# Kernel optimization log

Measured on AMD Instinct MI355X. Metric: run time of the kernel, lower is better.

The kernel has to match this reference:

```python
import jax, jax.numpy as jnp
import numpy as np

N_NODES = 100000
F_STATE = 64
HIDDEN = 256
N_EDGES = 1600000


def setup_inputs() -> dict:
    key = jax.random.key(0)
    ks = jax.random.split(key, 8)
    x = jax.random.normal(ks[0], (N_NODES, F_STATE), dtype=jnp.float32)
    edge_index = jax.random.randint(ks[1], (2, N_EDGES), 0, N_NODES, dtype=jnp.int32)
    # Pre-process MLP (1 layer): Dense(F_STATE -> HIDDEN), relu
    W_pre = jax.random.normal(ks[2], (F_STATE, HIDDEN), dtype=jnp.float32) / np.sqrt(F_STATE)
    b_pre = jnp.zeros((HIDDEN,), dtype=jnp.float32)
    # GeneralConv: Dense(HIDDEN -> HIDDEN), relu, then sum-aggregate message passing
    W_conv = jax.random.normal(ks[3], (HIDDEN, HIDDEN), dtype=jnp.float32) / np.sqrt(HIDDEN)
    b_conv = jnp.zeros((HIDDEN,), dtype=jnp.float32)
    # Post-process MLP (1 layer): Dense(2*HIDDEN -> F_STATE), activation=None
    W_post = jax.random.normal(ks[4], (2 * HIDDEN, F_STATE), dtype=jnp.float32) / np.sqrt(2 * HIDDEN)
    b_post = jnp.zeros((F_STATE,), dtype=jnp.float32)
    return {
        "x": x,
        "edge_index": edge_index,
        "W_pre": W_pre,
        "b_pre": b_pre,
        "W_conv": W_conv,
        "b_conv": b_conv,
        "W_post": W_post,
        "b_post": b_post,
        "steps": 4,
    }


def reference(x, edge_index, W_pre, b_pre, W_conv, b_conv, W_post, b_post, steps):
    n = x.shape[0]
    dst = edge_index[0]  # a.indices[:, 0] -> aggregation targets
    src = edge_index[1]  # a.indices[:, 1] -> message sources

    def step(h, _):
        p = jax.nn.relu(h @ W_pre + b_pre)                 # pre MLP     [N, H]
        m = jax.nn.relu(p @ W_conv + b_conv)               # conv dense  [N, H]
        z = jax.ops.segment_sum(m[src], dst, num_segments=n)  # sum agg  [N, H]
        out = jnp.concatenate([z, p], axis=-1) @ W_post + b_post  # cat-skip + post MLP (linear)
        return out, None

    out, _ = jax.lax.scan(step, x, None, length=steps)
    return out
```

## Files before the change

### kernel.cpp

```cpp
#include <hip/hip_runtime.h>


#define NN 100000
#define NPAD 100064
#define FS 64
#define HH 256
#define NE 1600000
#define NSTEPS 4
#define GA 128
#define EPB (NE / GA)
#define BK2SH 9
#define BS2 (1 << BK2SH)
#define NBK2 ((NN + BS2 - 1) / BS2)

typedef unsigned short u16;
typedef unsigned int u32;
typedef __attribute__((ext_vector_type(8))) short bfrag;
typedef __attribute__((ext_vector_type(4))) float ffrag;

static __device__ __forceinline__ u16 f2bf(float f) {
    union { float f; u32 u; } v; v.f = f;
    return (u16)((v.u + 0x7fffu + ((v.u >> 16) & 1u)) >> 16);
}
static __device__ __forceinline__ float bf2f(u16 h) {
    union { u32 u; float f; } v; v.u = (u32)h << 16; return v.f;
}
static __device__ __forceinline__ u32 pack2bf(float a, float b) {
    return (u32)f2bf(a) | ((u32)f2bf(b) << 16);
}

__global__ void cvt_x_k(const float4* __restrict__ x, uint2* __restrict__ hbf, int n4) {
    int i = blockIdx.x * 256 + threadIdx.x;
    if (i < n4) {
        float4 v = x[i];
        hbf[i] = make_uint2(pack2bf(v.x, v.y), pack2bf(v.z, v.w));
    }
}

__global__ void prep_w_k(const float* __restrict__ W_pre, const float* __restrict__ W_conv,
                         const float* __restrict__ W_post,
                         u16* __restrict__ Wpt, u16* __restrict__ Wct,
                         u16* __restrict__ Wzt, u16* __restrict__ Wp2t) {
    int i = blockIdx.x * 256 + threadIdx.x;
    if (i < 65536) {
        int c = i >> 8, k = i & 255;
        Wct[i] = f2bf(W_conv[k * HH + c]);
    } else if (i < 81920) {
        int j = i - 65536;
        int c = j >> 6, k = j & 63;
        Wpt[j] = f2bf(W_pre[k * HH + c]);
    } else if (i < 98304) {
        int j = i - 81920;
        int c = j >> 8, k = j & 255;
        Wzt[j] = f2bf(W_post[k * FS + c]);
    } else if (i < 114688) {
        int j = i - 98304;
        int c = j >> 8, k = j & 255;
        Wp2t[j] = f2bf(W_post[(HH + k) * FS + c]);
    }
}

__global__ __launch_bounds__(256) void fillA_k(const int* __restrict__ dst, const int* __restrict__ src,
                                               int* __restrict__ cntM, int* __restrict__ offM,
                                               u32* __restrict__ tmp) {
    __shared__ int cnt[256];
    __shared__ int sc[256];
    __shared__ int cur[256];
    const int t = threadIdx.x, b = blockIdx.x;
    const int e0 = b * EPB;
    cnt[t] = 0;
    __syncthreads();
    for (int i = t; i < EPB; i += 256) atomicAdd(&cnt[dst[e0 + i] >> BK2SH], 1);
    __syncthreads();
    int v = cnt[t];
    sc[t] = v;
    __syncthreads();
    for (int o = 1; o < 256; o <<= 1) {
        int y = (t >= o) ? sc[t - o] : 0;
        __syncthreads();
        sc[t] += y;
        __syncthreads();
    }
    int excl = sc[t] - v;
    cur[t] = excl;
    if (t < NBK2) {
        cntM[t * GA + b] = v;
        offM[t * GA + b] = excl;
    }
    __syncthreads();
    u32* seg = tmp + (size_t)b * EPB;
    for (int i = t; i < EPB; i += 256) {
        int d = dst[e0 + i], s = src[e0 + i];
        int pos = atomicAdd(&cur[d >> BK2SH], 1);
        seg[pos] = ((u32)(d & (BS2 - 1)) << 23) | (u32)s;
    }
}

__global__ void bscan_k(const int* __restrict__ cntM, int* __restrict__ bstart) {
    __shared__ int sh[256];
    const int t = threadIdx.x;
    int tot = 0;
    if (t < NBK2)
        for (int b = 0; b < GA; b++) tot += cntM[t * GA + b];
    sh[t] = tot;
    __syncthreads();
    for (int o = 1; o < 256; o <<= 1) {
        int y = (t >= o) ? sh[t - o] : 0;
        __syncthreads();
        sh[t] += y;
        __syncthreads();
    }
    if (t < NBK2) bstart[t] = sh[t] - tot;
    if (t == 255) bstart[NBK2] = sh[255];
}

__global__ __launch_bounds__(256) void fillB_k(const u32* __restrict__ tmp,
                                               const int* __restrict__ cntM, const int* __restrict__ offM,
                                               const int* __restrict__ bstart,
                                               int* __restrict__ offsets, int* __restrict__ srcs) {
    __shared__ int cnt[BS2];
    __shared__ int cur[BS2];
    __shared__ int runlen[GA];
    __shared__ int runoff[GA];
    const int t = threadIdx.x, k = blockIdx.x;
    const int nodeBase = k << BK2SH;
    cnt[t] = 0;
    cnt[t + 256] = 0;
    if (t < GA) {
        runlen[t] = cntM[k * GA + t];
        runoff[t] = offM[k * GA + t];
    }
    __syncthreads();
    const int rsub = t >> 6;
    const int elane = t & 63;
    for (int g = 0; g < GA / 4; g++) {
        int rb = g * 4 + rsub;
        int len = runlen[rb];
        const u32* run = tmp + (size_t)rb * EPB + runoff[rb];
        for (int e = elane; e < len; e += 64) atomicAdd(&cnt[run[e] >> 23], 1);
    }
    __syncthreads();
    int a = cnt[2 * t], b2 = cnt[2 * t + 1];
    int s = a + b2;
    cur[t] = s;
    __syncthreads();
    for (int o = 1; o < 256; o <<= 1) {
        int y = (t >= o) ? cur[t - o] : 0;
        __syncthreads();
        cur[t] += y;
        __syncthreads();
    }
    int exclPair = cur[t] - s;
    __syncthreads();
    const int base = bstart[k];
    int o0 = base + exclPair;
    int o1 = o0 + a;
    int n0 = nodeBase + 2 * t, n1 = n0 + 1;
    if (n0 < NN) offsets[n0] = o0;
    if (n1 < NN) offsets[n1] = o1;
    cur[2 * t] = o0;
    cur[2 * t + 1] = o1;
    __syncthreads();
    for (int g = 0; g < GA / 4; g++) {
        int rb = g * 4 + rsub;
        int len = runlen[rb];
        const u32* run = tmp + (size_t)rb * EPB + runoff[rb];
        for (int e = elane; e < len; e += 64) {
            u32 p = run[e];
            int pos = atomicAdd(&cur[p >> 23], 1);
            srcs[pos] = (int)(p & 0x7FFFFFu);
        }
    }
}

__global__ void final_off_k(int* __restrict__ offsets) {
    if (threadIdx.x == 0) offsets[NN] = NE;
}

__global__ __launch_bounds__(256, 4) void xform_k(const u16* __restrict__ hbf,
                                                  const u16* __restrict__ Wpt,
                                                  const float* __restrict__ b_pre,
                                                  const u16* __restrict__ Wct,
                                                  const float* __restrict__ b_conv,
                                                  const u16* __restrict__ Wzt,
                                                  const u16* __restrict__ Wp2t,
                                                  u16* __restrict__ qbf,
                                                  float* __restrict__ pw2o) {
    __shared__ u16 ts[64 * 264];
    const int t = threadIdx.x;
    const int wave = t >> 6, lane = t & 63;
    const int quad = lane >> 4, l16 = lane & 15;
    const int nodeBase = blockIdx.x * 64;

    {
        ffrag acc[4][4];
#pragma unroll
        for (int mt = 0; mt < 4; mt++)
#pragma unroll
            for (int nt = 0; nt < 4; nt++) acc[mt][nt] = (ffrag)0.f;
#pragma unroll
        for (int ch = 0; ch < 2; ch++) {
            const int kb = ch * 32 + quad * 8;
            bfrag a[4], b[4];
#pragma unroll
            for (int mt = 0; mt < 4; mt++)
                a[mt] = *(const bfrag*)(hbf + (size_t)(nodeBase + mt * 16 + l16) * FS + kb);
#pragma unroll
            for (int nt = 0; nt < 4; nt++)
                b[nt] = *(const bfrag*)(Wpt + (size_t)(wave * 64 + nt * 16 + l16) * FS + kb);
#pragma unroll
            for (int mt = 0; mt < 4; mt++)
#pragma unroll
                for (int nt = 0; nt < 4; nt++)
                    acc[mt][nt] = __builtin_amdgcn_mfma_f32_16x16x32_bf16(a[mt], b[nt], acc[mt][nt], 0, 0, 0);
        }
#pragma unroll
        for (int nt = 0; nt < 4; nt++) {
            const int col = wave * 64 + nt * 16 + l16;
            const float bv = b_pre[col];
#pragma unroll
            for (int mt = 0; mt < 4; mt++)
#pragma unroll
                for (int r = 0; r < 4; r++)
                    ts[(mt * 16 + quad * 4 + r) * 264 + col] = f2bf(fmaxf(acc[mt][nt][r] + bv, 0.f));
        }
    }
    __syncthreads();

    ffrag accm[4][4];
    ffrag accw[4];
    {
#pragma unroll
        for (int mt = 0; mt < 4; mt++) {
            accw[mt] = (ffrag)0.f;
#pragma unroll
            for (int nt = 0; nt < 4; nt++) accm[mt][nt] = (ffrag)0.f;
        }
#pragma unroll
        for (int ch = 0; ch < 8; ch++) {
            const int kb = ch * 32 + quad * 8;
            bfrag a[4], b[4], bw;
#pragma unroll
            for (int mt = 0; mt < 4; mt++)
                a[mt] = *(const bfrag*)(ts + (mt * 16 + l16) * 264 + kb);
#pragma unroll
            for (int nt = 0; nt < 4; nt++)
                b[nt] = *(const bfrag*)(Wct + (size_t)(wave * 64 + nt * 16 + l16) * HH + kb);
            bw = *(const bfrag*)(Wp2t + (size_t)(wave * 16 + l16) * HH + kb);
#pragma unroll
            for (int mt = 0; mt < 4; mt++) {
#pragma unroll
                for (int nt = 0; nt < 4; nt++)
                    accm[mt][nt] = __builtin_amdgcn_mfma_f32_16x16x32_bf16(a[mt], b[nt], accm[mt][nt], 0, 0, 0);
                accw[mt] = __builtin_amdgcn_mfma_f32_16x16x32_bf16(a[mt], bw, accw[mt], 0, 0, 0);
            }
        }
    }
    __syncthreads();

    {
#pragma unroll
        for (int nt = 0; nt < 4; nt++) {
            const int col = wave * 64 + nt * 16 + l16;
            const float bv = b_conv[col];
#pragma unroll
            for (int mt = 0; mt < 4; mt++)
#pragma unroll
                for (int r = 0; r < 4; r++)
                    ts[(mt * 16 + quad * 4 + r) * 264 + col] = f2bf(fmaxf(accm[mt][nt][r] + bv, 0.f));
        }
        const int colw = wave * 16 + l16;
#pragma unroll
        for (int mt = 0; mt < 4; mt++)
#pragma unroll
            for (int r = 0; r < 4; r++) {
                int node = nodeBase + mt * 16 + quad * 4 + r;
                if (node < NN) pw2o[(size_t)node * FS + colw] = accw[mt][r];
            }
    }
    __syncthreads();

    {
        ffrag qa[4];
#pragma unroll
        for (int mt = 0; mt < 4; mt++) qa[mt] = (ffrag)0.f;
#pragma unroll
        for (int ch = 0; ch < 8; ch++) {
            const int kb = ch * 32 + quad * 8;
            bfrag bz = *(const bfrag*)(Wzt + (size_t)(wave * 16 + l16) * HH + kb);
#pragma unroll
            for (int mt = 0; mt < 4; mt++) {
                bfrag am = *(const bfrag*)(ts + (mt * 16 + l16) * 264 + kb);
                qa[mt] = __builtin_amdgcn_mfma_f32_16x16x32_bf16(am, bz, qa[mt], 0, 0, 0);
            }
        }
        const int col = wave * 16 + l16;
#pragma unroll
        for (int mt = 0; mt < 4; mt++)
#pragma unroll
            for (int r = 0; r < 4; r++) {
                int node = nodeBase + mt * 16 + quad * 4 + r;
                if (node < NN) qbf[(size_t)node * FS + col] = f2bf(qa[mt][r]);
            }
    }
}

__global__ __launch_bounds__(256) void agg_k(const u32* __restrict__ q2,
                                             const int* __restrict__ offsets,
                                             const int* __restrict__ srcs,
                                             const float* __restrict__ pw2,
                                             const float* __restrict__ b_post,
                                             u32* __restrict__ hbf_out,
                                             float* __restrict__ outf) {
    const int wave = threadIdx.x >> 6;
    const int lane = threadIdx.x & 63;
    const int node = blockIdx.x * 4 + wave;
    const int half = lane >> 5, c = lane & 31;
    const int beg = offsets[node], end = offsets[node + 1];
    float ax = 0.f, ay = 0.f, bx = 0.f, by = 0.f;
    int e = beg + half;
    for (; e + 6 < end; e += 8) {
        int s0 = srcs[e], s1 = srcs[e + 2], s2 = srcs[e + 4], s3 = srcs[e + 6];
        u32 g0 = q2[(size_t)s0 * 32 + c];
        u32 g1 = q2[(size_t)s1 * 32 + c];
        u32 g2 = q2[(size_t)s2 * 32 + c];
        u32 g3 = q2[(size_t)s3 * 32 + c];
        ax += bf2f((u16)g0) + bf2f((u16)g1);
        ay += bf2f((u16)(g0 >> 16)) + bf2f((u16)(g1 >> 16));
        bx += bf2f((u16)g2) + bf2f((u16)g3);
        by += bf2f((u16)(g2 >> 16)) + bf2f((u16)(g3 >> 16));
    }
    for (; e < end; e += 2) {
        u32 g = q2[(size_t)srcs[e] * 32 + c];
        ax += bf2f((u16)g);
        ay += bf2f((u16)(g >> 16));
    }
    ax += bx; ay += by;
    ax += __shfl_xor(ax, 32);
    ay += __shfl_xor(ay, 32);
    if (half == 0) {
        float2 w = *(const float2*)&pw2[(size_t)node * FS + 2 * c];
        float2 b = *(const float2*)&b_post[2 * c];
        float hx = ax + w.x + b.x;
        float hy = ay + w.y + b.y;
        if (outf) {
            *(float2*)&outf[(size_t)node * FS + 2 * c] = make_float2(hx, hy);
        } else {
            hbf_out[(size_t)node * 32 + c] = pack2bf(hx, hy);
        }
    }
}

extern "C" void kernel_launch(void* const* d_in, const int* in_sizes, int n_in,
                              void* d_out, int out_size, void* d_ws, size_t ws_size,
                              hipStream_t stream) {
    const float* x      = (const float*)d_in[0];
    const int*   ei     = (const int*)d_in[1];
    const float* W_pre  = (const float*)d_in[2];
    const float* b_pre  = (const float*)d_in[3];
    const float* W_conv = (const float*)d_in[4];
    const float* b_conv = (const float*)d_in[5];
    const float* W_post = (const float*)d_in[6];
    const float* b_post = (const float*)d_in[7];
    float* out = (float*)d_out;

    char* ws = (char*)d_ws;
    size_t off = 0;
    auto alloc = [&](size_t bytes) -> char* {
        char* r = ws + off;
        off += (bytes + 255) & ~(size_t)255;
        return r;
    };
    u16* hbf     = (u16*)alloc((size_t)NPAD * FS * 2);
    u16* qbf     = (u16*)alloc((size_t)NN * FS * 2);
    float* pw2   = (float*)alloc((size_t)NPAD * FS * 4);
    u32* tmp     = (u32*)alloc((size_t)NE * 4);
    int* offsets = (int*)alloc((size_t)(NN + 1) * 4);
    int* srcs    = (int*)alloc((size_t)NE * 4);
    int* cntM    = (int*)alloc((size_t)NBK2 * GA * 4);
    int* offM    = (int*)alloc((size_t)NBK2 * GA * 4);
    int* bstart  = (int*)alloc((size_t)(NBK2 + 1) * 4);
    u16* Wpt     = (u16*)alloc((size_t)HH * FS * 2);
    u16* Wct     = (u16*)alloc((size_t)HH * HH * 2);
    u16* Wzt     = (u16*)alloc((size_t)FS * HH * 2);
    u16* Wp2t    = (u16*)alloc((size_t)FS * HH * 2);
    (void)ws_size; (void)in_sizes; (void)n_in; (void)out_size;

    const int* dst = ei;
    const int* src = ei + NE;

    cvt_x_k<<<(NN * FS / 4 + 255) / 256, 256, 0, stream>>>((const float4*)x, (uint2*)hbf, NN * FS / 4);
    prep_w_k<<<448, 256, 0, stream>>>(W_pre, W_conv, W_post, Wpt, Wct, Wzt, Wp2t);

    fillA_k<<<GA, 256, 0, stream>>>(dst, src, cntM, offM, tmp);
    bscan_k<<<1, 256, 0, stream>>>(cntM, bstart);
    fillB_k<<<NBK2, 256, 0, stream>>>(tmp, cntM, offM, bstart, offsets, srcs);
    final_off_k<<<1, 64, 0, stream>>>(offsets);

    const int GB = (NN + 63) / 64;
    for (int s = 0; s < NSTEPS; s++) {
        xform_k<<<GB, 256, 0, stream>>>(hbf, Wpt, b_pre, Wct, b_conv, Wzt, Wp2t, qbf, pw2);
        if (s < NSTEPS - 1)
            agg_k<<<NN / 4, 256, 0, stream>>>((const u32*)qbf, offsets, srcs, pw2, b_post,
                                              (u32*)hbf, nullptr);
        else
            agg_k<<<NN / 4, 256, 0, stream>>>((const u32*)qbf, offsets, srcs, pw2, b_post,
                                              nullptr, out);
    }
}
```

Baseline: 633.8 us.

## Stage xform outputs through LDS for coalesced stores, store pw2 as bf16, prefetch weights

Outputs of xform_k (the skip-path product and q) now go to LDS staging tiles first and are then written to global memory as coalesced 16-byte rows, where before each lane wrote a scattered 2- or 4-byte store. The skip-path intermediate pw2 is kept in bf16 rather than fp32, which halves its write and read traffic and costs a little precision. Weight fragments for the conv and Wz GEMMs are double-buffered in registers to hide global load latency. Launch bounds drop to 3 blocks per CU to make room for the extra registers and LDS, which lowers occupancy.

```diff
diff --git a/kernel.cpp b/kernel.cpp
--- a/kernel.cpp
+++ b/kernel.cpp
@@ -177,7 +177,7 @@
     if (threadIdx.x == 0) offsets[NN] = NE;
 }
 
-__global__ __launch_bounds__(256, 4) void xform_k(const u16* __restrict__ hbf,
+__global__ __launch_bounds__(256, 3) void xform_k(const u16* __restrict__ hbf,
                                                   const u16* __restrict__ Wpt,
                                                   const float* __restrict__ b_pre,
                                                   const u16* __restrict__ Wct,
@@ -185,8 +185,10 @@
                                                   const u16* __restrict__ Wzt,
                                                   const u16* __restrict__ Wp2t,
                                                   u16* __restrict__ qbf,
-                                                  float* __restrict__ pw2o) {
-    __shared__ u16 ts[64 * 264];
+                                                  u16* __restrict__ pw2o) {
+    __shared__ __align__(16) u16 ts[64 * 264];
+    __shared__ __align__(16) u16 stA[64 * 72];
+    __shared__ __align__(16) u16 stB[64 * 72];
     const int t = threadIdx.x;
     const int wave = t >> 6, lane = t & 63;
     const int quad = lane >> 4, l16 = lane & 15;
@@ -236,23 +238,35 @@
 #pragma unroll
             for (int nt = 0; nt < 4; nt++) accm[mt][nt] = (ffrag)0.f;
         }
+        bfrag b[2][4], bw[2];
+        {
+            const int kb0 = quad * 8;
+#pragma unroll
+            for (int nt = 0; nt < 4; nt++)
+                b[0][nt] = *(const bfrag*)(Wct + (size_t)(wave * 64 + nt * 16 + l16) * HH + kb0);
+            bw[0] = *(const bfrag*)(Wp2t + (size_t)(wave * 16 + l16) * HH + kb0);
+        }
 #pragma unroll
         for (int ch = 0; ch < 8; ch++) {
+            const int cur = ch & 1, nxt = cur ^ 1;
+            if (ch < 7) {
+                const int kb2 = (ch + 1) * 32 + quad * 8;
+#pragma unroll
+                for (int nt = 0; nt < 4; nt++)
+                    b[nxt][nt] = *(const bfrag*)(Wct + (size_t)(wave * 64 + nt * 16 + l16) * HH + kb2);
+                bw[nxt] = *(const bfrag*)(Wp2t + (size_t)(wave * 16 + l16) * HH + kb2);
+            }
             const int kb = ch * 32 + quad * 8;
-            bfrag a[4], b[4], bw;
+            bfrag a[4];
 #pragma unroll
             for (int mt = 0; mt < 4; mt++)
                 a[mt] = *(const bfrag*)(ts + (mt * 16 + l16) * 264 + kb);
 #pragma unroll
-            for (int nt = 0; nt < 4; nt++)
-                b[nt] = *(const bfrag*)(Wct + (size_t)(wave * 64 + nt * 16 + l16) * HH + kb);
-            bw = *(const bfrag*)(Wp2t + (size_t)(wave * 16 + l16) * HH + kb);
-#pragma unroll
             for (int mt = 0; mt < 4; mt++) {
 #pragma unroll
                 for (int nt = 0; nt < 4; nt++)
-                    accm[mt][nt] = __builtin_amdgcn_mfma_f32_16x16x32_bf16(a[mt], b[nt], accm[mt][nt], 0, 0, 0);
-                accw[mt] = __builtin_amdgcn_mfma_f32_16x16x32_bf16(a[mt], bw, accw[mt], 0, 0, 0);
+                    accm[mt][nt] = __builtin_amdgcn_mfma_f32_16x16x32_bf16(a[mt], b[cur][nt], accm[mt][nt], 0, 0, 0);
+                accw[mt] = __builtin_amdgcn_mfma_f32_16x16x32_bf16(a[mt], bw[cur], accw[mt], 0, 0, 0);
             }
         }
     }
@@ -273,42 +287,59 @@
 #pragma unroll
         for (int mt = 0; mt < 4; mt++)
 #pragma unroll
-            for (int r = 0; r < 4; r++) {
-                int node = nodeBase + mt * 16 + quad * 4 + r;
-                if (node < NN) pw2o[(size_t)node * FS + colw] = accw[mt][r];
-            }
-    }
-    __syncthreads();
+            for (int r = 0; r < 4; r++)
+                stA[(mt * 16 + quad * 4 + r) * 72 + colw] = f2bf(accw[mt][r]);
+    }
+    __syncthreads();
+
+#pragma unroll
+    for (int s = 0; s < 2; s++) {
+        const int j = t + s * 256;
+        const int row = j >> 3, seg = j & 7;
+        uint4 v = *(const uint4*)(stA + row * 72 + seg * 8);
+        *(uint4*)(pw2o + (size_t)(nodeBase + row) * FS + seg * 8) = v;
+    }
 
     {
         ffrag qa[4];
 #pragma unroll
         for (int mt = 0; mt < 4; mt++) qa[mt] = (ffrag)0.f;
+        bfrag bz[2];
+        bz[0] = *(const bfrag*)(Wzt + (size_t)(wave * 16 + l16) * HH + quad * 8);
 #pragma unroll
         for (int ch = 0; ch < 8; ch++) {
+            const int cur = ch & 1;
+            if (ch < 7)
+                bz[cur ^ 1] = *(const bfrag*)(Wzt + (size_t)(wave * 16 + l16) * HH + (ch + 1) * 32 + quad * 8);
             const int kb = ch * 32 + quad * 8;
-            bfrag bz = *(const bfrag*)(Wzt + (size_t)(wave * 16 + l16) * HH + kb);
 #pragma unroll
             for (int mt = 0; mt < 4; mt++) {
                 bfrag am = *(const bfrag*)(ts + (mt * 16 + l16) * 264 + kb);
-                qa[mt] = __builtin_amdgcn_mfma_f32_16x16x32_bf16(am, bz, qa[mt], 0, 0, 0);
+                qa[mt] = __builtin_amdgcn_mfma_f32_16x16x32_bf16(am, bz[cur], qa[mt], 0, 0, 0);
             }
         }
         const int col = wave * 16 + l16;
 #pragma unroll
         for (int mt = 0; mt < 4; mt++)
 #pragma unroll
-            for (int r = 0; r < 4; r++) {
-                int node = nodeBase + mt * 16 + quad * 4 + r;
-                if (node < NN) qbf[(size_t)node * FS + col] = f2bf(qa[mt][r]);
-            }
+            for (int r = 0; r < 4; r++)
+                stB[(mt * 16 + quad * 4 + r) * 72 + col] = f2bf(qa[mt][r]);
+    }
+    __syncthreads();
+
+#pragma unroll
+    for (int s = 0; s < 2; s++) {
+        const int j = t + s * 256;
+        const int row = j >> 3, seg = j & 7;
+        uint4 v = *(const uint4*)(stB + row * 72 + seg * 8);
+        *(uint4*)(qbf + (size_t)(nodeBase + row) * FS + seg * 8) = v;
     }
 }
 
 __global__ __launch_bounds__(256) void agg_k(const u32* __restrict__ q2,
                                              const int* __restrict__ offsets,
                                              const int* __restrict__ srcs,
-                                             const float* __restrict__ pw2,
+                                             const u32* __restrict__ pw2,
                                              const float* __restrict__ b_post,
                                              u32* __restrict__ hbf_out,
                                              float* __restrict__ outf) {
@@ -339,10 +370,10 @@
     ax += __shfl_xor(ax, 32);
     ay += __shfl_xor(ay, 32);
     if (half == 0) {
-        float2 w = *(const float2*)&pw2[(size_t)node * FS + 2 * c];
+        u32 wp = pw2[(size_t)node * 32 + c];
         float2 b = *(const float2*)&b_post[2 * c];
-        float hx = ax + w.x + b.x;
-        float hy = ay + w.y + b.y;
+        float hx = ax + bf2f((u16)wp) + b.x;
+        float hy = ay + bf2f((u16)(wp >> 16)) + b.y;
         if (outf) {
             *(float2*)&outf[(size_t)node * FS + 2 * c] = make_float2(hx, hy);
         } else {
@@ -372,8 +403,8 @@
         return r;
     };
     u16* hbf     = (u16*)alloc((size_t)NPAD * FS * 2);
-    u16* qbf     = (u16*)alloc((size_t)NN * FS * 2);
-    float* pw2   = (float*)alloc((size_t)NPAD * FS * 4);
+    u16* qbf     = (u16*)alloc((size_t)NPAD * FS * 2);
+    u16* pw2     = (u16*)alloc((size_t)NPAD * FS * 2);
     u32* tmp     = (u32*)alloc((size_t)NE * 4);
     int* offsets = (int*)alloc((size_t)(NN + 1) * 4);
     int* srcs    = (int*)alloc((size_t)NE * 4);
@@ -401,10 +432,10 @@
     for (int s = 0; s < NSTEPS; s++) {
         xform_k<<<GB, 256, 0, stream>>>(hbf, Wpt, b_pre, Wct, b_conv, Wzt, Wp2t, qbf, pw2);
         if (s < NSTEPS - 1)
-            agg_k<<<NN / 4, 256, 0, stream>>>((const u32*)qbf, offsets, srcs, pw2, b_post,
+            agg_k<<<NN / 4, 256, 0, stream>>>((const u32*)qbf, offsets, srcs, (const u32*)pw2, b_post,
                                               (u32*)hbf, nullptr);
         else
-            agg_k<<<NN / 4, 256, 0, stream>>>((const u32*)qbf, offsets, srcs, pw2, b_post,
+            agg_k<<<NN / 4, 256, 0, stream>>>((const u32*)qbf, offsets, srcs, (const u32*)pw2, b_post,
                                               nullptr, out);
     }
 }
```

Result: faster. 607.6 us (-4.1%).
